# Performance work log

Measured on AMD Instinct MI355X. Metric: run time of the kernel, lower is better.

Reference implementation:

```python
import jax, jax.numpy as jnp
import numpy as np

EMBED_DIM = 64


def _knn_graph(dist, k):
    """dist: [n, n]. Returns src [n,k], nbr [n,k], d [n,k] with self-edges removed,
    neighbors in ascending-distance order (matches torch.topk largest=False + self filter)."""
    n = dist.shape[0]
    _, idx = jax.lax.top_k(-dist, k + 1)  # [n, k+1] indices, ascending distance
    node = jnp.arange(n)[:, None]
    # stable reorder pushing the self index to the end, preserving distance order
    key = jnp.arange(k + 1)[None, :] + (k + 2) * (idx == node)
    order = jnp.argsort(key, axis=-1)
    nbr = jnp.take_along_axis(idx, order, axis=-1)[:, :k]  # [n, k]
    d = jnp.take_along_axis(dist, nbr, axis=-1)            # [n, k]
    src = jnp.broadcast_to(node, (n, k))
    return src, nbr, d


def setup_inputs() -> dict:
    key = jax.random.key(0)
    k1, k2, k3, k4 = jax.random.split(key, 4)
    B, n = 8, 1000
    locs = jax.random.uniform(k1, (B, n, 2), dtype=jnp.float32)
    init_embeddings = jax.random.normal(k2, (B, n, EMBED_DIM), dtype=jnp.float32)
    # nn.Linear(1, embed_dim): W [embed_dim, 1], b [embed_dim]
    W = jax.random.normal(k3, (EMBED_DIM, 1), dtype=jnp.float32)
    b = jax.random.normal(k4, (EMBED_DIM,), dtype=jnp.float32)
    return {"locs": locs, "init_embeddings": init_embeddings, "W": W, "b": b, "k_sparse": 200}


def reference(locs, init_embeddings, W, b, k_sparse):
    B, n, _ = locs.shape
    # cdist p=2: [B, n, n]
    diff = locs[:, :, None, :] - locs[:, None, :, :]
    dist = jnp.sqrt(jnp.sum(diff * diff, axis=-1))
    src, nbr, d = jax.vmap(lambda dm: _knn_graph(dm, k_sparse))(dist)  # [B, n, k]
    # Batch.from_data_list: concatenate graphs with node-index offsets
    off = (jnp.arange(B, dtype=src.dtype) * n)[:, None, None]
    edge_index = jnp.stack([(src + off).reshape(-1), (nbr + off).reshape(-1)], axis=0)  # [2, B*n*k]
    x = init_embeddings.reshape(B * n, -1)  # batch.x
    edge_attr = d.reshape(-1, 1)            # [E, 1]
    edge_emb = edge_attr @ W.T + b          # [E, embed_dim]
    return x, edge_index.astype(jnp.int32), edge_emb
```

## Files before the change

kernel.cpp:

```cpp
#include <hip/hip_runtime.h>
#include <stdint.h>

#define NNODE 1000
#define KSP   200
#define DIM   64
#define BATCH 8
#define WPB   4

__global__ __launch_bounds__(256) void knn_edge_kernel(
    const float* __restrict__ locs,
    const float* __restrict__ emb,
    const float* __restrict__ W,
    const float* __restrict__ bias,
    float* __restrict__ out)
{
    __shared__ int      hist[WPB][256];
    __shared__ uint64_t cand[WPB][256];
    __shared__ int      ssp[WPB];

    const int tid  = threadIdx.x;
    const int w    = tid >> 6;
    const int lane = tid & 63;
    const int node = blockIdx.x * WPB + w;
    const int b    = node / NNODE;
    const int i    = node - b * NNODE;

    #pragma unroll
    for (int c = 0; c < 4; ++c) hist[w][c * 64 + lane] = 0;
    if (lane == 0) ssp[w] = KSP + 1;
    __builtin_amdgcn_wave_barrier();

    const float2* loc = (const float2*)(locs + (size_t)b * NNODE * 2);
    const float2 self = loc[i];

    for (int j = lane; j < NNODE; j += 64) {
        float2 pt = loc[j];
        float dx = __fsub_rn(self.x, pt.x);
        float dy = __fsub_rn(self.y, pt.y);
        float d  = __fsqrt_rn(__fadd_rn(__fmul_rn(dx, dx), __fmul_rn(dy, dy)));
        int q = (int)(d * 180.0f);
        q = q > 255 ? 255 : q;
        atomicAdd(&hist[w][q], 1);
    }
    __builtin_amdgcn_wave_barrier();

    int base = 0, Bcand = 1 << 30;
    #pragma unroll
    for (int c = 0; c < 4; ++c) {
        int x  = hist[w][c * 64 + lane];
        int sc = x;
        #pragma unroll
        for (int off = 1; off < 64; off <<= 1) {
            int y = __shfl_up(sc, off, 64);
            if (lane >= off) sc += y;
        }
        int cum = sc + base;
        if (cum >= KSP + 1 && Bcand == (1 << 30)) Bcand = c * 64 + lane;
        hist[w][c * 64 + lane] = cum - x;
        base += __shfl(sc, 63, 64);
    }
    #pragma unroll
    for (int off = 32; off; off >>= 1) Bcand = min(Bcand, __shfl_xor(Bcand, off, 64));
    const int B = Bcand;
    __builtin_amdgcn_wave_barrier();

    for (int j = lane; j < NNODE; j += 64) {
        float2 pt = loc[j];
        float dx = __fsub_rn(self.x, pt.x);
        float dy = __fsub_rn(self.y, pt.y);
        float d  = __fsqrt_rn(__fadd_rn(__fmul_rn(dx, dx), __fmul_rn(dy, dy)));
        int q = (int)(d * 180.0f);
        q = q > 255 ? 255 : q;
        if (q <= B) {
            int slot = atomicAdd(&hist[w][q], 1);
            if (slot < 256)
                cand[w][slot] = ((uint64_t)__float_as_uint(d) << 32) | (uint32_t)j;
        }
    }
    __builtin_amdgcn_wave_barrier();

    const int cumB = min(hist[w][B], 256);

    uint64_t mykey[4];
    int      myrank[4];
    #pragma unroll
    for (int s = 0; s < 4; ++s) {
        int t = lane + s * 64;
        myrank[s] = KSP + 1;
        if (t < cumB) {
            uint64_t k = cand[w][t];
            float d = __uint_as_float((uint32_t)(k >> 32));
            int q = (int)(d * 180.0f);
            q = q > 255 ? 255 : q;
            int start = q ? hist[w][q - 1] : 0;
            int end   = min(hist[w][q], 256);
            int r = start;
            for (int m = start; m < end; ++m) {
                uint64_t kk = cand[w][m];
                r += (kk < k) ? 1 : 0;
            }
            mykey[s]  = k;
            myrank[s] = r;
        }
    }
    __builtin_amdgcn_wave_barrier();

    #pragma unroll
    for (int s = 0; s < 4; ++s) {
        int t = lane + s * 64;
        if (t < cumB) {
            int r = myrank[s];
            if (r <= KSP) cand[w][r] = mykey[s];
            if ((uint32_t)mykey[s] == (uint32_t)i) ssp[w] = r;
        }
    }
    __builtin_amdgcn_wave_barrier();
    const int sp = ssp[w];

    const size_t E = (size_t)BATCH * NNODE * KSP;
    float* x_out = out;
    float* ei0   = out + (size_t)BATCH * NNODE * DIM;
    float* ei1   = ei0 + E;
    float* eemb  = ei1 + E;

    x_out[(size_t)node * DIM + lane] = emb[(size_t)node * DIM + lane];

    const size_t ebase = (size_t)node * KSP;
    for (int t = lane; t < KSP; t += 64) {
        int slot = t + (t >= sp ? 1 : 0);
        uint64_t kk = cand[w][slot];
        ei0[ebase + t] = (float)node;
        ei1[ebase + t] = (float)(b * NNODE + (int)(uint32_t)kk);
    }

    const int c4 = (lane & 15) << 2;
    const float4 w4 = *(const float4*)(W + c4);
    const float4 b4 = *(const float4*)(bias + c4);
    float4* em4 = (float4*)(eemb + ebase * DIM);
    for (int t = lane; t < KSP * (DIM / 4); t += 64) {
        int e    = t >> 4;
        int slot = e + (e >= sp ? 1 : 0);
        float d = __uint_as_float((uint32_t)(cand[w][slot] >> 32));
        float4 v;
        v.x = fmaf(d, w4.x, b4.x);
        v.y = fmaf(d, w4.y, b4.y);
        v.z = fmaf(d, w4.z, b4.z);
        v.w = fmaf(d, w4.w, b4.w);
        em4[t] = v;
    }
}

extern "C" void kernel_launch(void* const* d_in, const int* in_sizes, int n_in,
                              void* d_out, int out_size, void* d_ws, size_t ws_size,
                              hipStream_t stream) {
    const float* locs = (const float*)d_in[0];
    const float* emb  = (const float*)d_in[1];
    const float* W    = (const float*)d_in[2];
    const float* bias = (const float*)d_in[3];
    float* out = (float*)d_out;

    knn_edge_kernel<<<(BATCH * NNODE) / WPB, 256, 0, stream>>>(locs, emb, W, bias, out);
}
```

Baseline: 101.8 us.

## Split kNN selection and edge output into producer/consumer warp pairs

Each block now holds producer waves, which run the histogram-based kNN selection, and consumer waves, which stream the edge-index and edge-embedding writes. Producers handle two nodes each and hand results over through an LDS ring guarded by a workgroup-scope release/acquire flag. Consumers write the x copy and ei0 early, then spin-wait per node. The intent is to overlap the compute-heavy selection with the store-bound output phase. The cost is extra LDS, spin-wait sleeps, and half the waves sitting idle while they wait.

```diff
diff --git a/kernel.cpp b/kernel.cpp
--- a/kernel.cpp
+++ b/kernel.cpp
@@ -5,117 +5,32 @@
 #define KSP   200
 #define DIM   64
 #define BATCH 8
-#define WPB   4
+#define NPAIR 4
+#define NPP   2
+#define NPB   (NPAIR * NPP)
+#define NBLK  (BATCH * NNODE / NPB)
 
-__global__ __launch_bounds__(256) void knn_edge_kernel(
+__global__ __launch_bounds__(512) void knn_pc_kernel(
     const float* __restrict__ locs,
     const float* __restrict__ emb,
     const float* __restrict__ W,
     const float* __restrict__ bias,
     float* __restrict__ out)
 {
-    __shared__ int      hist[WPB][256];
-    __shared__ uint64_t cand[WPB][256];
-    __shared__ int      ssp[WPB];
+    __shared__ int      hist[NPAIR][256];
+    __shared__ uint64_t cand[NPAIR][256];
+    __shared__ float    ring[NPAIR][NPP][2][KSP];
+    __shared__ int      prodSeq[NPAIR];
+    __shared__ int      ssp[NPAIR];
 
     const int tid  = threadIdx.x;
-    const int w    = tid >> 6;
+    const int wv   = tid >> 6;
     const int lane = tid & 63;
-    const int node = blockIdx.x * WPB + w;
-    const int b    = node / NNODE;
-    const int i    = node - b * NNODE;
+    const bool producer = (wv < NPAIR);
+    const int p = producer ? wv : wv - NPAIR;
 
-    #pragma unroll
-    for (int c = 0; c < 4; ++c) hist[w][c * 64 + lane] = 0;
-    if (lane == 0) ssp[w] = KSP + 1;
-    __builtin_amdgcn_wave_barrier();
-
-    const float2* loc = (const float2*)(locs + (size_t)b * NNODE * 2);
-    const float2 self = loc[i];
-
-    for (int j = lane; j < NNODE; j += 64) {
-        float2 pt = loc[j];
-        float dx = __fsub_rn(self.x, pt.x);
-        float dy = __fsub_rn(self.y, pt.y);
-        float d  = __fsqrt_rn(__fadd_rn(__fmul_rn(dx, dx), __fmul_rn(dy, dy)));
-        int q = (int)(d * 180.0f);
-        q = q > 255 ? 255 : q;
-        atomicAdd(&hist[w][q], 1);
-    }
-    __builtin_amdgcn_wave_barrier();
-
-    int base = 0, Bcand = 1 << 30;
-    #pragma unroll
-    for (int c = 0; c < 4; ++c) {
-        int x  = hist[w][c * 64 + lane];
-        int sc = x;
-        #pragma unroll
-        for (int off = 1; off < 64; off <<= 1) {
-            int y = __shfl_up(sc, off, 64);
-            if (lane >= off) sc += y;
-        }
-        int cum = sc + base;
-        if (cum >= KSP + 1 && Bcand == (1 << 30)) Bcand = c * 64 + lane;
-        hist[w][c * 64 + lane] = cum - x;
-        base += __shfl(sc, 63, 64);
-    }
-    #pragma unroll
-    for (int off = 32; off; off >>= 1) Bcand = min(Bcand, __shfl_xor(Bcand, off, 64));
-    const int B = Bcand;
-    __builtin_amdgcn_wave_barrier();
-
-    for (int j = lane; j < NNODE; j += 64) {
-        float2 pt = loc[j];
-        float dx = __fsub_rn(self.x, pt.x);
-        float dy = __fsub_rn(self.y, pt.y);
-        float d  = __fsqrt_rn(__fadd_rn(__fmul_rn(dx, dx), __fmul_rn(dy, dy)));
-        int q = (int)(d * 180.0f);
-        q = q > 255 ? 255 : q;
-        if (q <= B) {
-            int slot = atomicAdd(&hist[w][q], 1);
-            if (slot < 256)
-                cand[w][slot] = ((uint64_t)__float_as_uint(d) << 32) | (uint32_t)j;
-        }
-    }
-    __builtin_amdgcn_wave_barrier();
-
-    const int cumB = min(hist[w][B], 256);
-
-    uint64_t mykey[4];
-    int      myrank[4];
-    #pragma unroll
-    for (int s = 0; s < 4; ++s) {
-        int t = lane + s * 64;
-        myrank[s] = KSP + 1;
-        if (t < cumB) {
-            uint64_t k = cand[w][t];
-            float d = __uint_as_float((uint32_t)(k >> 32));
-            int q = (int)(d * 180.0f);
-            q = q > 255 ? 255 : q;
-            int start = q ? hist[w][q - 1] : 0;
-            int end   = min(hist[w][q], 256);
-            int r = start;
-            for (int m = start; m < end; ++m) {
-                uint64_t kk = cand[w][m];
-                r += (kk < k) ? 1 : 0;
-            }
-            mykey[s]  = k;
-            myrank[s] = r;
-        }
-    }
-    __builtin_amdgcn_wave_barrier();
-
-    #pragma unroll
-    for (int s = 0; s < 4; ++s) {
-        int t = lane + s * 64;
-        if (t < cumB) {
-            int r = myrank[s];
-            if (r <= KSP) cand[w][r] = mykey[s];
-            if ((uint32_t)mykey[s] == (uint32_t)i) ssp[w] = r;
-        }
-    }
-    __builtin_amdgcn_wave_barrier();
-    const int sp = ssp[w];
+    if (tid < NPAIR) prodSeq[tid] = 0;
+    __syncthreads();
 
     const size_t E = (size_t)BATCH * NNODE * KSP;
     float* x_out = out;
@@ -123,30 +38,150 @@
     float* ei1   = ei0 + E;
     float* eemb  = ei1 + E;
 
-    x_out[(size_t)node * DIM + lane] = emb[(size_t)node * DIM + lane];
+    if (producer) {
+        for (int m = 0; m < NPP; ++m) {
+            const int node = blockIdx.x * NPB + p * NPP + m;
+            const int b    = node / NNODE;
+            const int i    = node - b * NNODE;
 
-    const size_t ebase = (size_t)node * KSP;
-    for (int t = lane; t < KSP; t += 64) {
-        int slot = t + (t >= sp ? 1 : 0);
-        uint64_t kk = cand[w][slot];
-        ei0[ebase + t] = (float)node;
-        ei1[ebase + t] = (float)(b * NNODE + (int)(uint32_t)kk);
-    }
+            #pragma unroll
+            for (int c = 0; c < 4; ++c) hist[p][c * 64 + lane] = 0;
+            if (lane == 0) ssp[p] = KSP + 1;
+            __builtin_amdgcn_wave_barrier();
 
-    const int c4 = (lane & 15) << 2;
-    const float4 w4 = *(const float4*)(W + c4);
-    const float4 b4 = *(const float4*)(bias + c4);
-    float4* em4 = (float4*)(eemb + ebase * DIM);
-    for (int t = lane; t < KSP * (DIM / 4); t += 64) {
-        int e    = t >> 4;
-        int slot = e + (e >= sp ? 1 : 0);
-        float d = __uint_as_float((uint32_t)(cand[w][slot] >> 32));
-        float4 v;
-        v.x = fmaf(d, w4.x, b4.x);
-        v.y = fmaf(d, w4.y, b4.y);
-        v.z = fmaf(d, w4.z, b4.z);
-        v.w = fmaf(d, w4.w, b4.w);
-        em4[t] = v;
+            const float2* loc = (const float2*)(locs + (size_t)b * NNODE * 2);
+            const float2 self = loc[i];
+
+            for (int j = lane; j < NNODE; j += 64) {
+                float2 pt = loc[j];
+                float dx = __fsub_rn(self.x, pt.x);
+                float dy = __fsub_rn(self.y, pt.y);
+                float d  = __fsqrt_rn(__fadd_rn(__fmul_rn(dx, dx), __fmul_rn(dy, dy)));
+                int q = (int)(d * 180.0f);
+                q = q > 255 ? 255 : q;
+                atomicAdd(&hist[p][q], 1);
+            }
+            __builtin_amdgcn_wave_barrier();
+
+            int base = 0, Bcand = 1 << 30;
+            #pragma unroll
+            for (int c = 0; c < 4; ++c) {
+                int x  = hist[p][c * 64 + lane];
+                int sc = x;
+                #pragma unroll
+                for (int off = 1; off < 64; off <<= 1) {
+                    int y = __shfl_up(sc, off, 64);
+                    if (lane >= off) sc += y;
+                }
+                int cum = sc + base;
+                if (cum >= KSP + 1 && Bcand == (1 << 30)) Bcand = c * 64 + lane;
+                hist[p][c * 64 + lane] = cum - x;
+                base += __shfl(sc, 63, 64);
+            }
+            #pragma unroll
+            for (int off = 32; off; off >>= 1) Bcand = min(Bcand, __shfl_xor(Bcand, off, 64));
+            const int B = Bcand;
+            __builtin_amdgcn_wave_barrier();
+
+            for (int j = lane; j < NNODE; j += 64) {
+                float2 pt = loc[j];
+                float dx = __fsub_rn(self.x, pt.x);
+                float dy = __fsub_rn(self.y, pt.y);
+                float d  = __fsqrt_rn(__fadd_rn(__fmul_rn(dx, dx), __fmul_rn(dy, dy)));
+                int q = (int)(d * 180.0f);
+                q = q > 255 ? 255 : q;
+                if (q <= B) {
+                    int slot = atomicAdd(&hist[p][q], 1);
+                    if (slot < 256)
+                        cand[p][slot] = ((uint64_t)__float_as_uint(d) << 32) | (uint32_t)j;
+                }
+            }
+            __builtin_amdgcn_wave_barrier();
+
+            const int cumB = min(hist[p][B], 256);
+
+            uint64_t mykey[4];
+            int      myrank[4];
+            #pragma unroll
+            for (int s = 0; s < 4; ++s) {
+                int t = lane + s * 64;
+                myrank[s] = KSP + 1;
+                if (t < cumB) {
+                    uint64_t k = cand[p][t];
+                    float d = __uint_as_float((uint32_t)(k >> 32));
+                    int q = (int)(d * 180.0f);
+                    q = q > 255 ? 255 : q;
+                    int start = q ? hist[p][q - 1] : 0;
+                    int end   = min(hist[p][q], 256);
+                    int r = start;
+                    for (int mm = start; mm < end; ++mm)
+                        r += (cand[p][mm] < k) ? 1 : 0;
+                    mykey[s]  = k;
+                    myrank[s] = r;
+                }
+            }
+            #pragma unroll
+            for (int s = 0; s < 4; ++s) {
+                int t = lane + s * 64;
+                if (t < cumB && (uint32_t)mykey[s] == (uint32_t)i) ssp[p] = myrank[s];
+            }
+            __builtin_amdgcn_wave_barrier();
+            const int sp = ssp[p];
+
+            #pragma unroll
+            for (int s = 0; s < 4; ++s) {
+                int t = lane + s * 64;
+                if (t < cumB) {
+                    int r = myrank[s];
+                    if (r <= KSP && r != sp) {
+                        int tt = r - (r > sp ? 1 : 0);
+                        ring[p][m][0][tt] = __uint_as_float((uint32_t)(mykey[s] >> 32));
+                        ring[p][m][1][tt] = (float)(b * NNODE + (int)(uint32_t)mykey[s]);
+                    }
+                }
+            }
+            __threadfence_block();
+            if (lane == 0)
+                __hip_atomic_store(&prodSeq[p], m + 1, __ATOMIC_RELEASE,
+                                   __HIP_MEMORY_SCOPE_WORKGROUP);
+            __builtin_amdgcn_wave_barrier();
+        }
+    } else {
+        const int c4 = (lane & 15) << 2;
+        const float4 w4 = *(const float4*)(W + c4);
+        const float4 b4 = *(const float4*)(bias + c4);
+
+        #pragma unroll
+        for (int m = 0; m < NPP; ++m) {
+            const int node = blockIdx.x * NPB + p * NPP + m;
+            x_out[(size_t)node * DIM + lane] = emb[(size_t)node * DIM + lane];
+            const size_t ebase = (size_t)node * KSP;
+            for (int t = lane; t < KSP; t += 64) ei0[ebase + t] = (float)node;
+        }
+
+        for (int m = 0; m < NPP; ++m) {
+            const int node = blockIdx.x * NPB + p * NPP + m;
+            const size_t ebase = (size_t)node * KSP;
+
+            while (__hip_atomic_load(&prodSeq[p], __ATOMIC_ACQUIRE,
+                                     __HIP_MEMORY_SCOPE_WORKGROUP) <= m)
+                __builtin_amdgcn_s_sleep(8);
+
+            for (int t = lane; t < KSP; t += 64)
+                ei1[ebase + t] = ring[p][m][1][t];
+
+            float4* em4 = (float4*)(eemb + ebase * DIM);
+            for (int t = lane; t < KSP * (DIM / 4); t += 64) {
+                int e = t >> 4;
+                float d = ring[p][m][0][e];
+                float4 v;
+                v.x = fmaf(d, w4.x, b4.x);
+                v.y = fmaf(d, w4.y, b4.y);
+                v.z = fmaf(d, w4.z, b4.z);
+                v.w = fmaf(d, w4.w, b4.w);
+                em4[t] = v;
+            }
+        }
     }
 }
 
@@ -159,5 +194,5 @@
     const float* bias = (const float*)d_in[3];
     float* out = (float*)d_out;
 
-    knn_edge_kernel<<<(BATCH * NNODE) / WPB, 256, 0, stream>>>(locs, emb, W, bias, out);
+    knn_pc_kernel<<<NBLK, 512, 0, stream>>>(locs, emb, W, bias, out);
 }
```

Result: slower. 130.5 us (+28.2%).

## Stage batch locations in LDS, widen blocks, restructure histogram scan

Applied to the files above, without the earlier changes.

Doubles the waves per block to 8 and has the block cooperatively load its batch's 1000 point locations into shared memory, so distance passes read LDS instead of global memory. The histogram prefix scan is rewritten to do one wave-level scan over int4 chunks instead of four separate scans. Output writes that don't depend on the kNN result (x copy, source indices) are moved earlier to overlap with compute. The trade-off is a block barrier and more shared memory per block, which may reduce occupancy.

```diff
diff --git a/kernel.cpp b/kernel.cpp
--- a/kernel.cpp
+++ b/kernel.cpp
@@ -5,15 +5,17 @@
 #define KSP   200
 #define DIM   64
 #define BATCH 8
-#define WPB   4
+#define WPB   8
+#define NBLK  (BATCH * NNODE / WPB)
 
-__global__ __launch_bounds__(256) void knn_edge_kernel(
+__global__ __launch_bounds__(512) void knn_edge_kernel(
     const float* __restrict__ locs,
     const float* __restrict__ emb,
     const float* __restrict__ W,
     const float* __restrict__ bias,
     float* __restrict__ out)
 {
+    __shared__ float4   sloc4[NNODE / 2];
     __shared__ int      hist[WPB][256];
     __shared__ uint64_t cand[WPB][256];
     __shared__ int      ssp[WPB];
@@ -25,16 +27,31 @@
     const int b    = node / NNODE;
     const int i    = node - b * NNODE;
 
-    #pragma unroll
-    for (int c = 0; c < 4; ++c) hist[w][c * 64 + lane] = 0;
-    if (lane == 0) ssp[w] = KSP + 1;
-    __builtin_amdgcn_wave_barrier();
+    if (tid < NNODE / 2) sloc4[tid] = ((const float4*)(locs + (size_t)b * NNODE * 2))[tid];
+    ((int4*)hist)[tid] = make_int4(0, 0, 0, 0);
+    if (tid < WPB) ssp[tid] = KSP + 1;
+    __syncthreads();
 
-    const float2* loc = (const float2*)(locs + (size_t)b * NNODE * 2);
-    const float2 self = loc[i];
+    const float2* sloc = (const float2*)sloc4;
+    const float2 self = sloc[i];
+
+    const size_t E = (size_t)BATCH * NNODE * KSP;
+    float* x_out = out;
+    float* ei0   = out + (size_t)BATCH * NNODE * DIM;
+    float* ei1   = ei0 + E;
+    float* eemb  = ei1 + E;
+
+    const int c4 = (lane & 15) << 2;
+    const float4 w4 = *(const float4*)(W + c4);
+    const float4 b4 = *(const float4*)(bias + c4);
+
+    x_out[(size_t)node * DIM + lane] = emb[(size_t)node * DIM + lane];
+    const size_t ebase = (size_t)node * KSP;
+    const float fnode = (float)node;
+    for (int t = lane; t < KSP; t += 64) ei0[ebase + t] = fnode;
 
     for (int j = lane; j < NNODE; j += 64) {
-        float2 pt = loc[j];
+        float2 pt = sloc[j];
         float dx = __fsub_rn(self.x, pt.x);
         float dy = __fsub_rn(self.y, pt.y);
         float d  = __fsqrt_rn(__fadd_rn(__fmul_rn(dx, dx), __fmul_rn(dy, dy)));
@@ -44,28 +61,36 @@
     }
     __builtin_amdgcn_wave_barrier();
 
-    int base = 0, Bcand = 1 << 30;
+    int4 h4 = ((int4*)&hist[w][0])[lane];
+    int s0 = h4.x;
+    int s1 = s0 + h4.y;
+    int s2 = s1 + h4.z;
+    int s3 = s2 + h4.w;
+    int sc = s3;
     #pragma unroll
-    for (int c = 0; c < 4; ++c) {
-        int x  = hist[w][c * 64 + lane];
-        int sc = x;
-        #pragma unroll
-        for (int off = 1; off < 64; off <<= 1) {
-            int y = __shfl_up(sc, off, 64);
-            if (lane >= off) sc += y;
-        }
-        int cum = sc + base;
-        if (cum >= KSP + 1 && Bcand == (1 << 30)) Bcand = c * 64 + lane;
-        hist[w][c * 64 + lane] = cum - x;
-        base += __shfl(sc, 63, 64);
+    for (int off = 1; off < 64; off <<= 1) {
+        int y = __shfl_up(sc, off, 64);
+        if (lane >= off) sc += y;
     }
+    const int excl = sc - s3;
+    int bc = 1 << 30;
+    if      (excl + s0 >= KSP + 1) bc = 4 * lane;
+    else if (excl + s1 >= KSP + 1) bc = 4 * lane + 1;
+    else if (excl + s2 >= KSP + 1) bc = 4 * lane + 2;
+    else if (excl + s3 >= KSP + 1) bc = 4 * lane + 3;
     #pragma unroll
-    for (int off = 32; off; off >>= 1) Bcand = min(Bcand, __shfl_xor(Bcand, off, 64));
-    const int B = Bcand;
+    for (int off = 32; off; off >>= 1) bc = min(bc, __shfl_xor(bc, off, 64));
+    const int B = bc;
+    int4 st;
+    st.x = excl;
+    st.y = excl + s0;
+    st.z = excl + s1;
+    st.w = excl + s2;
+    ((int4*)&hist[w][0])[lane] = st;
     __builtin_amdgcn_wave_barrier();
 
     for (int j = lane; j < NNODE; j += 64) {
-        float2 pt = loc[j];
+        float2 pt = sloc[j];
         float dx = __fsub_rn(self.x, pt.x);
         float dy = __fsub_rn(self.y, pt.y);
         float d  = __fsqrt_rn(__fadd_rn(__fmul_rn(dx, dx), __fmul_rn(dy, dy)));
@@ -95,10 +120,8 @@
             int start = q ? hist[w][q - 1] : 0;
             int end   = min(hist[w][q], 256);
             int r = start;
-            for (int m = start; m < end; ++m) {
-                uint64_t kk = cand[w][m];
-                r += (kk < k) ? 1 : 0;
-            }
+            for (int m = start; m < end; ++m)
+                r += (cand[w][m] < k) ? 1 : 0;
             mykey[s]  = k;
             myrank[s] = r;
         }
@@ -117,25 +140,12 @@
     __builtin_amdgcn_wave_barrier();
     const int sp = ssp[w];
 
-    const size_t E = (size_t)BATCH * NNODE * KSP;
-    float* x_out = out;
-    float* ei0   = out + (size_t)BATCH * NNODE * DIM;
-    float* ei1   = ei0 + E;
-    float* eemb  = ei1 + E;
-
-    x_out[(size_t)node * DIM + lane] = emb[(size_t)node * DIM + lane];
-
-    const size_t ebase = (size_t)node * KSP;
     for (int t = lane; t < KSP; t += 64) {
         int slot = t + (t >= sp ? 1 : 0);
         uint64_t kk = cand[w][slot];
-        ei0[ebase + t] = (float)node;
         ei1[ebase + t] = (float)(b * NNODE + (int)(uint32_t)kk);
     }
 
-    const int c4 = (lane & 15) << 2;
-    const float4 w4 = *(const float4*)(W + c4);
-    const float4 b4 = *(const float4*)(bias + c4);
     float4* em4 = (float4*)(eemb + ebase * DIM);
     for (int t = lane; t < KSP * (DIM / 4); t += 64) {
         int e    = t >> 4;
@@ -159,5 +169,5 @@
     const float* bias = (const float*)d_in[3];
     float* out = (float*)d_out;
 
-    knn_edge_kernel<<<(BATCH * NNODE) / WPB, 256, 0, stream>>>(locs, emb, W, bias, out);
+    knn_edge_kernel<<<NBLK, 512, 0, stream>>>(locs, emb, W, bias, out);
 }
```

After: 93.38 us. -8.3%, faster.
